# Kernel tuning notes

Hardware: AMD Instinct MI355X
Metric: run time of the kernel (lower is better)

## Reference

```python
import jax, jax.numpy as jnp
import numpy as np

EMBED_DIM = 1024
HEADS = 16
HEAD_DIM = EMBED_DIM // HEADS
N, SEQ = 2, 2048


def setup_inputs() -> dict:
    key = jax.random.key(0)
    ks = jax.random.split(key, 9)
    s = 1.0 / np.sqrt(HEAD_DIM)
    inp = {
        "values": jax.random.normal(ks[0], (N, SEQ, EMBED_DIM), jnp.float32),
        "keys": jax.random.normal(ks[1], (N, SEQ, EMBED_DIM), jnp.float32),
        "query": jax.random.normal(ks[2], (N, SEQ, EMBED_DIM), jnp.float32),
        "mask": jax.random.randint(ks[3], (N, 1, SEQ, SEQ), 0, 2, jnp.int32),
        # per-head projection weights (torch Linear: y = x @ W.T)
        "Wv": jax.random.normal(ks[4], (HEAD_DIM, HEAD_DIM), jnp.float32) * s,
        "Wk": jax.random.normal(ks[5], (HEAD_DIM, HEAD_DIM), jnp.float32) * s,
        "Wq": jax.random.normal(ks[6], (HEAD_DIM, HEAD_DIM), jnp.float32) * s,
        "Wo": jax.random.normal(ks[7], (EMBED_DIM, EMBED_DIM), jnp.float32) * (1.0 / np.sqrt(EMBED_DIM)),
        "bo": jax.random.normal(ks[8], (EMBED_DIM,), jnp.float32) * 0.01,
    }
    return inp


def reference(values, keys, query, mask, Wv, Wk, Wq, Wo, bo):
    n, q_len = query.shape[0], query.shape[1]
    v_len, k_len = values.shape[1], keys.shape[1]
    # reshape to [N, len, H, D]
    v = values.reshape(n, v_len, HEADS, HEAD_DIM)
    k = keys.reshape(n, k_len, HEADS, HEAD_DIM)
    q = query.reshape(n, q_len, HEADS, HEAD_DIM)
    # per-head linear projections (shared weight across heads), torch: x @ W.T
    v = jnp.einsum("nlhd,ed->nlhe", v, Wv)
    k = jnp.einsum("nlhd,ed->nlhe", k, Wk)
    q = jnp.einsum("nlhd,ed->nlhe", q, Wq)
    # energy: [N, H, Q, K]
    energy = jnp.einsum("nqhd,nkhd->nhqk", q, k)
    energy = jnp.where(mask == 0, jnp.float32(-1e20), energy)
    # NOTE: original scales by sqrt(embed_dim), not sqrt(head_dim)
    attention = jax.nn.softmax(energy / jnp.sqrt(jnp.float32(EMBED_DIM)), axis=3)
    out = jnp.einsum("nhql,nlhd->nqhd", attention, v).reshape(n, q_len, EMBED_DIM)
    out = out @ Wo.T + bo  # fc_out; dropout is identity in eval mode
    return out
```

## Files before the change

kernel.cpp:

```cpp
#include <hip/hip_runtime.h>
#include <hip/hip_bf16.h>

#define NB 2
#define SEQ 2048
#define HEADS 16
#define HD 64
#define ED 1024

typedef __bf16 bf16x8 __attribute__((ext_vector_type(8)));
typedef float f32x4 __attribute__((ext_vector_type(4)));
typedef unsigned short u16x8 __attribute__((ext_vector_type(8)));
typedef unsigned short u16x4 __attribute__((ext_vector_type(4)));

#if __has_builtin(__builtin_amdgcn_exp2f)
#define EXP2(x) __builtin_amdgcn_exp2f(x)
#else
#define EXP2(x) __builtin_exp2f(x)
#endif

__device__ __forceinline__ unsigned short f2bf(float f) {
    unsigned u = __builtin_bit_cast(unsigned, f);
    u += 0x7fffu + ((u >> 16) & 1u);
    return (unsigned short)(u >> 16);
}

__device__ __forceinline__ bf16x8 cvt8(const float* __restrict__ p) {
    const float4* p4 = (const float4*)p;
    float4 a = p4[0], b = p4[1];
    u16x8 u;
    u[0] = f2bf(a.x); u[1] = f2bf(a.y); u[2] = f2bf(a.z); u[3] = f2bf(a.w);
    u[4] = f2bf(b.x); u[5] = f2bf(b.y); u[6] = f2bf(b.z); u[7] = f2bf(b.w);
    return __builtin_bit_cast(bf16x8, u);
}

__device__ __forceinline__ bf16x8 ldfrag(const void* p) {
    uint4 v = *(const uint4*)p;
    return __builtin_bit_cast(bf16x8, v);
}

__device__ __forceinline__ f32x4 mfma16(bf16x8 a, bf16x8 b, f32x4 c) {
    return __builtin_amdgcn_mfma_f32_16x16x32_bf16(a, b, c, 0, 0, 0);
}

__device__ __forceinline__ unsigned packbf(float lo, float hi) {
    unsigned a = __builtin_bit_cast(unsigned, hi) + 0x8000u;
    unsigned b = __builtin_bit_cast(unsigned, lo) + 0x8000u;
    return __builtin_amdgcn_perm(a, b, 0x07060302u);
}

#define GLOAD_LDS(gp, lp) \
    __builtin_amdgcn_global_load_lds( \
        (const __attribute__((address_space(1))) unsigned int*)(gp), \
        (__attribute__((address_space(3))) unsigned int*)(lp), 16, 0, 0)

#define QSCALE 0.04508422f

__global__ __launch_bounds__(256) void proj_prep_kernel(
    const float* __restrict__ qin, const float* __restrict__ kin, const float* __restrict__ vin,
    const float* __restrict__ Wq, const float* __restrict__ Wk, const float* __restrict__ Wv,
    unsigned short* __restrict__ Qb, unsigned short* __restrict__ Kb,
    unsigned short* __restrict__ Vt,
    const int* __restrict__ mask, unsigned long long* __restrict__ bits,
    const float* __restrict__ Wo, unsigned short* __restrict__ Wob)
{
    __shared__ __align__(16) char tile[64 * 144];

    int bid = blockIdx.x;
    if (bid >= 3072) {
        int b2 = bid - 3072;
        if (b2 < NB * SEQ * SEQ / 256) {
            size_t i = (size_t)b2 * 256 + threadIdx.x;
            int m = mask[i];
            unsigned long long b = __ballot(m != 0);
            if ((threadIdx.x & 63) == 0) bits[i >> 6] = b;
        } else {
            size_t i = ((size_t)(b2 - NB * SEQ * SEQ / 256) * 256 + threadIdx.x) * 4;
            float4 v = *(const float4*)(Wo + i);
            u16x4 u;
            u[0] = f2bf(v.x); u[1] = f2bf(v.y); u[2] = f2bf(v.z); u[3] = f2bf(v.w);
            *(u16x4*)(Wob + i) = u;
        }
        return;
    }

    int t3  = bid >> 10;
    int rem = bid & 1023;
    int h   = rem >> 6;
    int rt  = rem & 63;
    int wave = threadIdx.x >> 6, lane = threadIdx.x & 63;
    int quad = lane >> 4, l16 = lane & 15;

    const float* in = (t3 == 0) ? qin : ((t3 == 1) ? kin : vin);
    const float* W  = (t3 == 0) ? Wq  : ((t3 == 1) ? Wk  : Wv);

    int r0 = rt * 64 + wave * 16;

    bf16x8 bf0[4], bf1[4];
#pragma unroll
    for (int sl = 0; sl < 4; ++sl) {
        const float* wrow = W + (sl * 16 + l16) * 64;
        bf0[sl] = cvt8(wrow + quad * 8);
        bf1[sl] = cvt8(wrow + 32 + quad * 8);
    }
    const float* xrow = in + (size_t)(r0 + l16) * ED + h * 64;
    bf16x8 af0 = cvt8(xrow + quad * 8);
    bf16x8 af1 = cvt8(xrow + 32 + quad * 8);

    f32x4 acc[4];
#pragma unroll
    for (int sl = 0; sl < 4; ++sl) {
        f32x4 c = {0.f, 0.f, 0.f, 0.f};
        c = mfma16(af0, bf0[sl], c);
        c = mfma16(af1, bf1[sl], c);
        acc[sl] = c;
    }
    float sc = (t3 == 0) ? QSCALE : 1.0f;

    size_t nh = (size_t)((r0 >> 11) * HEADS + h);
    int rl = lane >> 3, cl = lane & 7;

    if (t3 != 2) {
#pragma unroll
        for (int r = 0; r < 4; ++r) {
            int srow = wave * 16 + quad * 4 + r;
#pragma unroll
            for (int sl = 0; sl < 4; ++sl)
                *(unsigned short*)(tile + srow * 144 + (sl * 16 + l16) * 2) =
                    f2bf(acc[sl][r] * sc);
        }
        unsigned short* dst = (t3 == 0) ? Qb : Kb;
        int s0 = (r0 & 2047);
#pragma unroll
        for (int g = 0; g < 2; ++g) {
            int lrow = wave * 16 + g * 8 + rl;
            uint4 v = *(const uint4*)(tile + lrow * 144 + cl * 16);
            *(uint4*)(dst + (nh * SEQ + (s0 & ~15) + g * 8 + rl) * HD + cl * 8) = v;
        }
    } else {
#pragma unroll
        for (int r = 0; r < 4; ++r) {
            int srow = wave * 16 + quad * 4 + r;
#pragma unroll
            for (int sl = 0; sl < 4; ++sl)
                *(unsigned short*)(tile + (sl * 16 + l16) * 144 + srow * 2) =
                    f2bf(acc[sl][r]);
        }
        __syncthreads();
        int s_tile = rt & 31;
#pragma unroll
        for (int g = 0; g < 2; ++g) {
            int erow = wave * 16 + g * 8 + rl;
            uint4 v = *(const uint4*)(tile + erow * 144 + cl * 16);
            *(uint4*)(Vt + ((nh * 32 + s_tile) * 64 + erow) * 64 + cl * 8) = v;
        }
    }
}

template <int SPLIT>
__global__ __launch_bounds__(256, 4) void attn_kernel(
    const unsigned short* __restrict__ Qb, const unsigned short* __restrict__ Kb,
    const unsigned short* __restrict__ Vt2, const unsigned long long* __restrict__ mb,
    unsigned short* __restrict__ Ab, float* __restrict__ Of, float* __restrict__ Ls)
{
    __shared__ __align__(16) char smem[24576 + 4 * 2304];

    int tid = threadIdx.x;
    int wave = tid >> 6, lane = tid & 63;
    int quad = lane >> 4, l16 = lane & 15;

    int b   = blockIdx.x;
    int xcd = b & 7;
    int j   = b >> 3;
    int nh, qb, half;
    if (SPLIT) { nh = xcd * 4 + (j >> 5); int r = j & 31; qb = r >> 1; half = r & 1; }
    else       { nh = xcd * 4 + (j >> 4); qb = j & 15; half = 0; }
    int n = nh >> 4, h = nh & 15;
    int q0 = qb * 128 + wave * 32;

    size_t headoff = (size_t)nh * SEQ * HD;
    bf16x8 qf[2][2];
#pragma unroll
    for (int t = 0; t < 2; ++t) {
        const unsigned short* qrow = Qb + headoff + (size_t)(q0 + t * 16 + l16) * HD;
        qf[t][0] = ldfrag(qrow + quad * 8);
        qf[t][1] = ldfrag(qrow + 32 + quad * 8);
    }

    int srow = lane >> 3, sslot = lane & 7;
    int stoff = srow * 128 + (((sslot - srow) & 7) * 16);

    int rotA = ((quad + l16) & 7) * 16;
    int aK0 = l16 * 128 + rotA;
    int aV  = 16384 + l16 * 128 + rotA;
    int aVx = aV ^ 64;
    char* pbase = smem + 24576 + wave * 2304;
    char* pw = pbase + l16 * 144 + quad * 8;
    char* pr = pbase + l16 * 144 + quad * 16;

    const unsigned short* gK = Kb + headoff;
    const unsigned short* gV = Vt2 + (size_t)nh * (32 * 4096);
    const unsigned long long* mbase = mb + (size_t)n * (SEQ * SEQ / 64)
                                         + (size_t)(q0 + l16) * (SEQ / 64);

    u16x8 ou;
#pragma unroll
    for (int jj = 0; jj < 8; ++jj) ou[jj] = 0x3F80;
    bf16x8 ones = __builtin_bit_cast(bf16x8, ou);

    f32x4 o[2][4] = {{{0,0,0,0},{0,0,0,0},{0,0,0,0},{0,0,0,0}},
                     {{0,0,0,0},{0,0,0,0},{0,0,0,0},{0,0,0,0}}};
    f32x4 lacc[2] = {{0,0,0,0},{0,0,0,0}};
    int qsh = quad * 4;

    int kb0   = SPLIT ? half * (SEQ / 2) : 0;
    int kbend = SPLIT ? kb0 + (SEQ / 2) : SEQ;

    {
        const char* sK = (const char*)(gK + (size_t)kb0 * 64) + stoff;
        const char* sV = (const char*)(gV + (size_t)(kb0 >> 6) * 4096) + stoff;
#pragma unroll
        for (int i2 = 0; i2 < 2; ++i2) {
            int c = wave * 2 + i2;
            GLOAD_LDS(sK + c * 1024, smem + c * 1024);
            GLOAD_LDS(sV + c * 1024, smem + 16384 + c * 1024);
        }
    }

    int par = 0;
    for (int kb = kb0; kb < kbend; kb += 64) {
        int kbn = (kb + 64) & (SEQ - 1);
        __syncthreads();
        {
            const char* sK = (const char*)(gK + (size_t)kbn * 64) + stoff;
            char* dK = smem + (par ^ 1) * 8192;
#pragma unroll
            for (int i2 = 0; i2 < 2; ++i2) {
                int c = wave * 2 + i2;
                GLOAD_LDS(sK + c * 1024, dK + c * 1024);
            }
        }
        unsigned long long m64[2];
#pragma unroll
        for (int t = 0; t < 2; ++t)
            m64[t] = mbase[(size_t)(t * 16) * (SEQ / 64) + (kb >> 6)] >> qsh;

        const char* kbuf = smem + par * 8192;
        bf16x8 kf[4][2];
#pragma unroll
        for (int kt = 0; kt < 4; ++kt) {
            kf[kt][0] = ldfrag(kbuf + aK0 + kt * 2048);
            kf[kt][1] = ldfrag(kbuf + (aK0 ^ 64) + kt * 2048);
        }
#pragma unroll
        for (int t = 0; t < 2; ++t) {
            f32x4 c[4];
#pragma unroll
            for (int kt = 0; kt < 4; ++kt) {
                f32x4 cc = {0.f, 0.f, 0.f, 0.f};
                cc = mfma16(kf[kt][0], qf[t][0], cc);
                cc = mfma16(kf[kt][1], qf[t][1], cc);
                c[kt] = cc;
            }
            unsigned mlo = (unsigned)m64[t];
            unsigned mhi = (unsigned)(m64[t] >> 32);
#pragma unroll
            for (int kt = 0; kt < 4; ++kt) {
                unsigned mw = (kt & 2) ? mhi : mlo;
                int bs = (kt & 1) ? 16 : 0;
                float p0 = ((mw >> (bs + 0)) & 1u) ? EXP2(c[kt][0]) : 0.f;
                float p1 = ((mw >> (bs + 1)) & 1u) ? EXP2(c[kt][1]) : 0.f;
                float p2 = ((mw >> (bs + 2)) & 1u) ? EXP2(c[kt][2]) : 0.f;
                float p3 = ((mw >> (bs + 3)) & 1u) ? EXP2(c[kt][3]) : 0.f;
                uint2 dw = { packbf(p0, p1), packbf(p2, p3) };
                *(uint2*)(pw + kt * 32) = dw;
            }
            bf16x8 pb0 = ldfrag(pr);
            bf16x8 pb1 = ldfrag(pr + 64);
            lacc[t] = mfma16(ones, pb0, lacc[t]);
            lacc[t] = mfma16(ones, pb1, lacc[t]);
#pragma unroll
            for (int sl = 0; sl < 4; ++sl) {
                o[t][sl] = mfma16(ldfrag(smem + aV  + sl * 2048), pb0, o[t][sl]);
                o[t][sl] = mfma16(ldfrag(smem + aVx + sl * 2048), pb1, o[t][sl]);
            }
        }
        __syncthreads();
        {
            const char* sV = (const char*)(gV + (size_t)(kbn >> 6) * 4096) + stoff;
#pragma unroll
            for (int i2 = 0; i2 < 2; ++i2) {
                int c = wave * 2 + i2;
                GLOAD_LDS(sV + c * 1024, smem + 16384 + c * 1024);
            }
        }
        par ^= 1;
    }

#pragma unroll
    for (int t = 0; t < 2; ++t) {
        float s = lacc[t][0];
        int q = q0 + t * 16 + l16;
        if (SPLIT) {
            size_t qg = (size_t)nh * SEQ + q;
            if (quad == 0) Ls[(size_t)half * 65536 + qg] = s;
            float* op = Of + ((size_t)half * 65536 + qg) * 64 + qsh;
#pragma unroll
            for (int sl = 0; sl < 4; ++sl) {
                float4 v = { o[t][sl][0], o[t][sl][1], o[t][sl][2], o[t][sl][3] };
                *(float4*)(op + sl * 16) = v;
            }
        } else {
            float rinv = 1.0f / s;
            unsigned short* op = Ab + (((size_t)(n * SEQ + q)) * HEADS + h) * HD + qsh;
#pragma unroll
            for (int sl = 0; sl < 4; ++sl) {
                u16x4 u;
                u[0] = f2bf(o[t][sl][0] * rinv);
                u[1] = f2bf(o[t][sl][1] * rinv);
                u[2] = f2bf(o[t][sl][2] * rinv);
                u[3] = f2bf(o[t][sl][3] * rinv);
                *(u16x4*)(op + sl * 16) = u;
            }
        }
    }
}

__global__ __launch_bounds__(256) void combine_kernel(
    const float* __restrict__ Of, const float* __restrict__ Ls,
    unsigned short* __restrict__ Ab)
{
    int idx = blockIdx.x * 256 + threadIdx.x;
    int q  = idx >> 4;
    int d0 = (idx & 15) * 4;
    const float4 o0 = *(const float4*)(Of + (size_t)q * 64 + d0);
    const float4 o1 = *(const float4*)(Of + 4194304 + (size_t)q * 64 + d0);
    float rl = 1.0f / (Ls[q] + Ls[65536 + q]);
    int n = q >> 15, h = (q >> 11) & 15, s = q & 2047;
    size_t ab = (((size_t)(n * SEQ + s)) * HEADS + h) * HD + d0;
    u16x4 u;
    u[0] = f2bf((o0.x + o1.x) * rl);
    u[1] = f2bf((o0.y + o1.y) * rl);
    u[2] = f2bf((o0.z + o1.z) * rl);
    u[3] = f2bf((o0.w + o1.w) * rl);
    *(u16x4*)(Ab + ab) = u;
}

__global__ __launch_bounds__(256) void out_gemm_kernel(
    const unsigned short* __restrict__ Ab, const unsigned short* __restrict__ Wob,
    const float* __restrict__ bo, float* __restrict__ out)
{
    __shared__ __align__(16) char lds[49152];

    int tid = threadIdx.x;
    int wave = tid >> 6, lane = tid & 63;
    int quad = lane >> 4, l16 = lane & 15;
    int rt = blockIdx.x >> 4, ct = blockIdx.x & 15;
    int wr = wave >> 1, wc = wave & 1;

    int srow = lane >> 3, sslot = lane & 7;
    int stoff = srow * 2048 + (((sslot - srow) & 7) * 16);
    const char* gA = (const char*)Ab  + (size_t)rt * 128 * 2048 + stoff;
    const char* gB = (const char*)Wob + (size_t)ct * 64 * 2048 + stoff;

    int aA[4], aB[2];
#pragma unroll
    for (int i = 0; i < 4; ++i) {
        int rowA = wr * 64 + i * 16 + l16;
        aA[i] = rowA * 128 + (((quad + rowA) & 7) * 16);
    }
#pragma unroll
    for (int sl = 0; sl < 2; ++sl) {
        int rowB = wc * 32 + sl * 16 + l16;
        aB[sl] = rowB * 128 + (((quad + rowB) & 7) * 16);
    }

#pragma unroll
    for (int i = 0; i < 4; ++i) {
        int c = wave * 4 + i;
        GLOAD_LDS(gA + (size_t)c * 16384, lds + c * 1024);
    }
#pragma unroll
    for (int i = 0; i < 2; ++i) {
        int c = wave * 2 + i;
        GLOAD_LDS(gB + (size_t)c * 16384, lds + 32768 + c * 1024);
    }

    f32x4 acc[4][2] = {};
    int par = 0;
    for (int f = 0; f < ED; f += 64) {
        int fn = (f + 64) & (ED - 1);
        __syncthreads();
        {
            int pA = (par ^ 1) * 16384;
            int pB = 32768 + (par ^ 1) * 8192;
#pragma unroll
            for (int i = 0; i < 4; ++i) {
                int c = wave * 4 + i;
                GLOAD_LDS(gA + (size_t)c * 16384 + fn * 2, lds + pA + c * 1024);
            }
#pragma unroll
            for (int i = 0; i < 2; ++i) {
                int c = wave * 2 + i;
                GLOAD_LDS(gB + (size_t)c * 16384 + fn * 2, lds + pB + c * 1024);
            }
        }
        int bA = par * 16384;
        int bB = 32768 + par * 8192;
#pragma unroll
        for (int kk = 0; kk < 2; ++kk) {
            int x = kk * 64;
            bf16x8 af[4], bfr[2];
#pragma unroll
            for (int i = 0; i < 4; ++i)    af[i]  = ldfrag(lds + bA + (aA[i] ^ x));
#pragma unroll
            for (int sl = 0; sl < 2; ++sl) bfr[sl] = ldfrag(lds + bB + (aB[sl] ^ x));
#pragma unroll
            for (int i = 0; i < 4; ++i)
#pragma unroll
                for (int sl = 0; sl < 2; ++sl)
                    acc[i][sl] = mfma16(af[i], bfr[sl], acc[i][sl]);
        }
        par ^= 1;
    }

    float bv[2];
#pragma unroll
    for (int sl = 0; sl < 2; ++sl)
        bv[sl] = bo[ct * 64 + wc * 32 + sl * 16 + l16];
#pragma unroll
    for (int i = 0; i < 4; ++i)
#pragma unroll
        for (int r = 0; r < 4; ++r) {
            int row = rt * 128 + wr * 64 + i * 16 + quad * 4 + r;
#pragma unroll
            for (int sl = 0; sl < 2; ++sl) {
                int e = ct * 64 + wc * 32 + sl * 16 + l16;
                out[(size_t)row * ED + e] = acc[i][sl][r] + bv[sl];
            }
        }
}

extern "C" void kernel_launch(void* const* d_in, const int* in_sizes, int n_in,
                              void* d_out, int out_size, void* d_ws, size_t ws_size,
                              hipStream_t stream)
{
    const float* values = (const float*)d_in[0];
    const float* keys   = (const float*)d_in[1];
    const float* query  = (const float*)d_in[2];
    const int*   mask   = (const int*)d_in[3];
    const float* Wv     = (const float*)d_in[4];
    const float* Wk     = (const float*)d_in[5];
    const float* Wq     = (const float*)d_in[6];
    const float* Wo     = (const float*)d_in[7];
    const float* bo     = (const float*)d_in[8];
    float* out = (float*)d_out;

    char* w = (char*)d_ws;
    unsigned short* Qb  = (unsigned short*)(w);
    unsigned short* Kb  = (unsigned short*)(w +  8388608);
    unsigned short* Vt  = (unsigned short*)(w + 16777216);
    unsigned short* Ab  = (unsigned short*)(w + 25165824);
    unsigned long long* Mb = (unsigned long long*)(w + 33554432);
    unsigned short* Wob = (unsigned short*)(w + 34603008);
    float* Of = (float*)(w + 36700160);
    float* Ls = (float*)(w + 70254592);

    bool split = ws_size >= 70778880ULL;

    proj_prep_kernel<<<3072 + NB * SEQ * SEQ / 256 + ED * ED / 1024, 256, 0, stream>>>(
        query, keys, values, Wq, Wk, Wv, Qb, Kb, Vt, mask, Mb, Wo, Wob);
    if (split) {
        attn_kernel<1><<<1024, 256, 0, stream>>>(Qb, Kb, Vt, Mb, Ab, Of, Ls);
        combine_kernel<<<4096, 256, 0, stream>>>(Of, Ls, Ab);
    } else {
        attn_kernel<0><<<512, 256, 0, stream>>>(Qb, Kb, Vt, Mb, Ab, Of, Ls);
    }
    out_gemm_kernel<<<512, 256, 0, stream>>>(Ab, Wob, bo, out);
}
```

Baseline: 234.5 us.

## Replace split-K attention with smaller query tiles per block over full key range

Drops the split-KV scheme, which wrote fp32 partial outputs and row sums and then merged them in a separate combine kernel. Each block now handles 64 queries (16 per wave) over all 2048 keys and normalizes in place, keeping the same 1024-block grid. This removes the fp32 partial round trip through memory and one kernel launch. In exchange, each K/V tile loaded into LDS is reused across half as many queries, so K/V load traffic per unit of compute doubles and there is less MFMA work per barrier.

After: 231.4 us. Within noise of the previous version (-1.3%).

```diff
diff --git a/kernel.cpp b/kernel.cpp
--- a/kernel.cpp
+++ b/kernel.cpp
@@ -156,11 +156,10 @@
     }
 }
 
-template <int SPLIT>
 __global__ __launch_bounds__(256, 4) void attn_kernel(
     const unsigned short* __restrict__ Qb, const unsigned short* __restrict__ Kb,
     const unsigned short* __restrict__ Vt2, const unsigned long long* __restrict__ mb,
-    unsigned short* __restrict__ Ab, float* __restrict__ Of, float* __restrict__ Ls)
+    unsigned short* __restrict__ Ab)
 {
     __shared__ __align__(16) char smem[24576 + 4 * 2304];
 
@@ -171,20 +170,15 @@
     int b   = blockIdx.x;
     int xcd = b & 7;
     int j   = b >> 3;
-    int nh, qb, half;
-    if (SPLIT) { nh = xcd * 4 + (j >> 5); int r = j & 31; qb = r >> 1; half = r & 1; }
-    else       { nh = xcd * 4 + (j >> 4); qb = j & 15; half = 0; }
+    int nh  = xcd * 4 + (j >> 5);
+    int qb  = j & 31;
     int n = nh >> 4, h = nh & 15;
-    int q0 = qb * 128 + wave * 32;
+    int q0 = qb * 64 + wave * 16;
 
     size_t headoff = (size_t)nh * SEQ * HD;
-    bf16x8 qf[2][2];
-#pragma unroll
-    for (int t = 0; t < 2; ++t) {
-        const unsigned short* qrow = Qb + headoff + (size_t)(q0 + t * 16 + l16) * HD;
-        qf[t][0] = ldfrag(qrow + quad * 8);
-        qf[t][1] = ldfrag(qrow + 32 + quad * 8);
-    }
+    const unsigned short* qrow = Qb + headoff + (size_t)(q0 + l16) * HD;
+    bf16x8 qf0 = ldfrag(qrow + quad * 8);
+    bf16x8 qf1 = ldfrag(qrow + 32 + quad * 8);
 
     int srow = lane >> 3, sslot = lane & 7;
     int stoff = srow * 128 + (((sslot - srow) & 7) * 16);
@@ -207,17 +201,13 @@
     for (int jj = 0; jj < 8; ++jj) ou[jj] = 0x3F80;
     bf16x8 ones = __builtin_bit_cast(bf16x8, ou);
 
-    f32x4 o[2][4] = {{{0,0,0,0},{0,0,0,0},{0,0,0,0},{0,0,0,0}},
-                     {{0,0,0,0},{0,0,0,0},{0,0,0,0},{0,0,0,0}}};
-    f32x4 lacc[2] = {{0,0,0,0},{0,0,0,0}};
+    f32x4 o[4] = {{0,0,0,0},{0,0,0,0},{0,0,0,0},{0,0,0,0}};
+    f32x4 lacc = {0,0,0,0};
     int qsh = quad * 4;
 
-    int kb0   = SPLIT ? half * (SEQ / 2) : 0;
-    int kbend = SPLIT ? kb0 + (SEQ / 2) : SEQ;
-
     {
-        const char* sK = (const char*)(gK + (size_t)kb0 * 64) + stoff;
-        const char* sV = (const char*)(gV + (size_t)(kb0 >> 6) * 4096) + stoff;
+        const char* sK = (const char*)gK + stoff;
+        const char* sV = (const char*)gV + stoff;
 #pragma unroll
         for (int i2 = 0; i2 < 2; ++i2) {
             int c = wave * 2 + i2;
@@ -227,7 +217,7 @@
     }
 
     int par = 0;
-    for (int kb = kb0; kb < kbend; kb += 64) {
+    for (int kb = 0; kb < SEQ; kb += 64) {
         int kbn = (kb + 64) & (SEQ - 1);
         __syncthreads();
         {
@@ -239,10 +229,7 @@
                 GLOAD_LDS(sK + c * 1024, dK + c * 1024);
             }
         }
-        unsigned long long m64[2];
-#pragma unroll
-        for (int t = 0; t < 2; ++t)
-            m64[t] = mbase[(size_t)(t * 16) * (SEQ / 64) + (kb >> 6)] >> qsh;
+        unsigned long long m64 = mbase[kb >> 6] >> qsh;
 
         const char* kbuf = smem + par * 8192;
         bf16x8 kf[4][2];
@@ -251,38 +238,35 @@
             kf[kt][0] = ldfrag(kbuf + aK0 + kt * 2048);
             kf[kt][1] = ldfrag(kbuf + (aK0 ^ 64) + kt * 2048);
         }
-#pragma unroll
-        for (int t = 0; t < 2; ++t) {
-            f32x4 c[4];
-#pragma unroll
-            for (int kt = 0; kt < 4; ++kt) {
-                f32x4 cc = {0.f, 0.f, 0.f, 0.f};
-                cc = mfma16(kf[kt][0], qf[t][0], cc);
-                cc = mfma16(kf[kt][1], qf[t][1], cc);
-                c[kt] = cc;
-            }
-            unsigned mlo = (unsigned)m64[t];
-            unsigned mhi = (unsigned)(m64[t] >> 32);
-#pragma unroll
-            for (int kt = 0; kt < 4; ++kt) {
-                unsigned mw = (kt & 2) ? mhi : mlo;
-                int bs = (kt & 1) ? 16 : 0;
-                float p0 = ((mw >> (bs + 0)) & 1u) ? EXP2(c[kt][0]) : 0.f;
-                float p1 = ((mw >> (bs + 1)) & 1u) ? EXP2(c[kt][1]) : 0.f;
-                float p2 = ((mw >> (bs + 2)) & 1u) ? EXP2(c[kt][2]) : 0.f;
-                float p3 = ((mw >> (bs + 3)) & 1u) ? EXP2(c[kt][3]) : 0.f;
-                uint2 dw = { packbf(p0, p1), packbf(p2, p3) };
-                *(uint2*)(pw + kt * 32) = dw;
-            }
-            bf16x8 pb0 = ldfrag(pr);
-            bf16x8 pb1 = ldfrag(pr + 64);
-            lacc[t] = mfma16(ones, pb0, lacc[t]);
-            lacc[t] = mfma16(ones, pb1, lacc[t]);
-#pragma unroll
-            for (int sl = 0; sl < 4; ++sl) {
-                o[t][sl] = mfma16(ldfrag(smem + aV  + sl * 2048), pb0, o[t][sl]);
-                o[t][sl] = mfma16(ldfrag(smem + aVx + sl * 2048), pb1, o[t][sl]);
-            }
+        f32x4 c[4];
+#pragma unroll
+        for (int kt = 0; kt < 4; ++kt) {
+            f32x4 cc = {0.f, 0.f, 0.f, 0.f};
+            cc = mfma16(kf[kt][0], qf0, cc);
+            cc = mfma16(kf[kt][1], qf1, cc);
+            c[kt] = cc;
+        }
+        unsigned mlo = (unsigned)m64;
+        unsigned mhi = (unsigned)(m64 >> 32);
+#pragma unroll
+        for (int kt = 0; kt < 4; ++kt) {
+            unsigned mw = (kt & 2) ? mhi : mlo;
+            int bs = (kt & 1) ? 16 : 0;
+            float p0 = ((mw >> (bs + 0)) & 1u) ? EXP2(c[kt][0]) : 0.f;
+            float p1 = ((mw >> (bs + 1)) & 1u) ? EXP2(c[kt][1]) : 0.f;
+            float p2 = ((mw >> (bs + 2)) & 1u) ? EXP2(c[kt][2]) : 0.f;
+            float p3 = ((mw >> (bs + 3)) & 1u) ? EXP2(c[kt][3]) : 0.f;
+            uint2 dw = { packbf(p0, p1), packbf(p2, p3) };
+            *(uint2*)(pw + kt * 32) = dw;
+        }
+        bf16x8 pb0 = ldfrag(pr);
+        bf16x8 pb1 = ldfrag(pr + 64);
+        lacc = mfma16(ones, pb0, lacc);
+        lacc = mfma16(ones, pb1, lacc);
+#pragma unroll
+        for (int sl = 0; sl < 4; ++sl) {
+            o[sl] = mfma16(ldfrag(smem + aV  + sl * 2048), pb0, o[sl]);
+            o[sl] = mfma16(ldfrag(smem + aVx + sl * 2048), pb1, o[sl]);
         }
         __syncthreads();
         {
@@ -296,53 +280,20 @@
         par ^= 1;
     }
 
-#pragma unroll
-    for (int t = 0; t < 2; ++t) {
-        float s = lacc[t][0];
-        int q = q0 + t * 16 + l16;
-        if (SPLIT) {
-            size_t qg = (size_t)nh * SEQ + q;
-            if (quad == 0) Ls[(size_t)half * 65536 + qg] = s;
-            float* op = Of + ((size_t)half * 65536 + qg) * 64 + qsh;
-#pragma unroll
-            for (int sl = 0; sl < 4; ++sl) {
-                float4 v = { o[t][sl][0], o[t][sl][1], o[t][sl][2], o[t][sl][3] };
-                *(float4*)(op + sl * 16) = v;
-            }
-        } else {
-            float rinv = 1.0f / s;
-            unsigned short* op = Ab + (((size_t)(n * SEQ + q)) * HEADS + h) * HD + qsh;
-#pragma unroll
-            for (int sl = 0; sl < 4; ++sl) {
-                u16x4 u;
-                u[0] = f2bf(o[t][sl][0] * rinv);
-                u[1] = f2bf(o[t][sl][1] * rinv);
-                u[2] = f2bf(o[t][sl][2] * rinv);
-                u[3] = f2bf(o[t][sl][3] * rinv);
-                *(u16x4*)(op + sl * 16) = u;
-            }
-        }
-    }
-}
-
-__global__ __launch_bounds__(256) void combine_kernel(
-    const float* __restrict__ Of, const float* __restrict__ Ls,
-    unsigned short* __restrict__ Ab)
-{
-    int idx = blockIdx.x * 256 + threadIdx.x;
-    int q  = idx >> 4;
-    int d0 = (idx & 15) * 4;
-    const float4 o0 = *(const float4*)(Of + (size_t)q * 64 + d0);
-    const float4 o1 = *(const float4*)(Of + 4194304 + (size_t)q * 64 + d0);
-    float rl = 1.0f / (Ls[q] + Ls[65536 + q]);
-    int n = q >> 15, h = (q >> 11) & 15, s = q & 2047;
-    size_t ab = (((size_t)(n * SEQ + s)) * HEADS + h) * HD + d0;
-    u16x4 u;
-    u[0] = f2bf((o0.x + o1.x) * rl);
-    u[1] = f2bf((o0.y + o1.y) * rl);
-    u[2] = f2bf((o0.z + o1.z) * rl);
-    u[3] = f2bf((o0.w + o1.w) * rl);
-    *(u16x4*)(Ab + ab) = u;
+    {
+        float rinv = 1.0f / lacc[0];
+        int q = q0 + l16;
+        unsigned short* op = Ab + (((size_t)(n * SEQ + q)) * HEADS + h) * HD + qsh;
+#pragma unroll
+        for (int sl = 0; sl < 4; ++sl) {
+            u16x4 u;
+            u[0] = f2bf(o[sl][0] * rinv);
+            u[1] = f2bf(o[sl][1] * rinv);
+            u[2] = f2bf(o[sl][2] * rinv);
+            u[3] = f2bf(o[sl][3] * rinv);
+            *(u16x4*)(op + sl * 16) = u;
+        }
+    }
 }
 
 __global__ __launch_bounds__(256) void out_gemm_kernel(
@@ -462,18 +413,9 @@
     unsigned short* Ab  = (unsigned short*)(w + 25165824);
     unsigned long long* Mb = (unsigned long long*)(w + 33554432);
     unsigned short* Wob = (unsigned short*)(w + 34603008);
-    float* Of = (float*)(w + 36700160);
-    float* Ls = (float*)(w + 70254592);
-
-    bool split = ws_size >= 70778880ULL;
 
     proj_prep_kernel<<<3072 + NB * SEQ * SEQ / 256 + ED * ED / 1024, 256, 0, stream>>>(
         query, keys, values, Wq, Wk, Wv, Qb, Kb, Vt, mask, Mb, Wo, Wob);
-    if (split) {
-        attn_kernel<1><<<1024, 256, 0, stream>>>(Qb, Kb, Vt, Mb, Ab, Of, Ls);
-        combine_kernel<<<4096, 256, 0, stream>>>(Of, Ls, Ab);
-    } else {
-        attn_kernel<0><<<512, 256, 0, stream>>>(Qb, Kb, Vt, Mb, Ab, Of, Ls);
-    }
+    attn_kernel<<<1024, 256, 0, stream>>>(Qb, Kb, Vt, Mb, Ab);
     out_gemm_kernel<<<512, 256, 0, stream>>>(Ab, Wob, bo, out);
 }
```
